# Performance work log

Measured on AMD Instinct MI355X. Metric: run time of the kernel, lower is better.

Reference implementation:

```python
import jax, jax.numpy as jnp
import numpy as np

IN_FEATURES = 512
DIM_EXPLOSION = 20
OUT_FEATURES = IN_FEATURES * DIM_EXPLOSION  # 10240
NB_PROJ_ENTRIES = 6
HASH_LENGTH = 32
BATCH = 4096


def _make_sparse_proj(key):
    """Sparse binary random projection: each of the OUT_FEATURES rows has
    NB_PROJ_ENTRIES entries set to 1 (as in OlfactoryModel.create_rand_proj_matrix)."""
    idx = jax.random.randint(key, (OUT_FEATURES, NB_PROJ_ENTRIES), 0, IN_FEATURES)
    rows = jnp.arange(OUT_FEATURES)[:, None]
    W = jnp.zeros((OUT_FEATURES, IN_FEATURES), dtype=jnp.float32)
    return W.at[rows, idx].set(1.0)


def setup_inputs() -> dict:
    key = jax.random.key(0)
    k1, k2 = jax.random.split(key)
    inp = jax.random.uniform(k1, (BATCH, IN_FEATURES), dtype=jnp.float32)
    W = _make_sparse_proj(k2)
    return {"input": inp, "weight": W, "hash_length": HASH_LENGTH}


def reference(input, weight, hash_length):
    # F.linear: [B, in] @ [out, in]^T -> [B, out]
    x = jnp.einsum('bi,oi->bo', input, weight)
    # MB_sparsify: winner-take-all, keep top `hash_length` activations per row, zero the rest
    topv = jax.lax.top_k(x, hash_length)[0]          # [B, k]
    thresh = topv[:, -1:]                            # k-th largest per row
    return jnp.where(x >= thresh, x, jnp.zeros_like(x))
```

## Files before the change

kernel.cpp:

```cpp
#include <hip/hip_runtime.h>


typedef float f4 __attribute__((ext_vector_type(4)));

constexpr int IN_F   = 512;
constexpr int OUT_F  = 10240;
constexpr int TPB    = 1024;
constexpr int ROWS   = 4;
constexpr int FPT    = OUT_F / TPB;
constexpr int NBINS  = 1024;
constexpr int CHUNK  = 8;
constexpr int NCHUNK = NBINS / CHUNK;
constexpr int NWAVES = TPB / 64;
constexpr int CAP    = 64;

__global__ __launch_bounds__(256) void extract_idx(const float* __restrict__ W,
                                                   uint4* __restrict__ packed,
                                                   int out_f) {
  int row  = blockIdx.x * 4 + (threadIdx.x >> 6);
  int lane = threadIdx.x & 63;
  if (row >= out_f) return;

  const float* wr = W + (size_t)row * IN_F;
  unsigned long long masks[8];
#pragma unroll
  for (int c = 0; c < 8; ++c) {
    float v = wr[c * 64 + lane];
    masks[c] = __ballot(v != 0.0f);
  }
  if (lane == 0) {
    unsigned idx[6] = {IN_F, IN_F, IN_F, IN_F, IN_F, IN_F};
    int n = 0;
#pragma unroll
    for (int c = 0; c < 8; ++c) {
      unsigned long long m = masks[c];
      while (m && n < 6) {
        int b = __builtin_ctzll(m);
        idx[n++] = (unsigned)(c * 64 + b);
        m &= m - 1;
      }
    }
    uint4 r;
    r.x = idx[0] | (idx[1] << 16);
    r.y = idx[2] | (idx[3] << 16);
    r.z = idx[4] | (idx[5] << 16);
    r.w = (unsigned)n;
    packed[row] = r;
  }
}

__device__ __forceinline__ float row_val(const f4* in4, uint4 p, int r) {
  const float* b = (const float*)in4;
  float s = b[(p.x & 0xFFFFu) * 4 + r];
  s += b[(p.x >> 16) * 4 + r];
  s += b[(p.y & 0xFFFFu) * 4 + r];
  s += b[(p.y >> 16) * 4 + r];
  s += b[(p.z & 0xFFFFu) * 4 + r];
  s += b[(p.z >> 16) * 4 + r];
  return s;
}

__global__ __launch_bounds__(TPB, 4) void fly_hash(const float* __restrict__ inp,
                                                   const uint4* __restrict__ packed,
                                                   const int* __restrict__ kptr,
                                                   float* __restrict__ out) {
  __shared__ f4    in4[IN_F + 1];
  __shared__ int   hist[ROWS * NBINS];
  __shared__ int   csum[ROWS * NCHUNK];
  __shared__ int   wsum[NWAVES];
  __shared__ int   sh_bstar[ROWS], sh_above[ROWS], sh_n[ROWS], sh_cnt[ROWS];
  __shared__ float sh_list[ROWS][CAP];
  __shared__ float sh_thr[ROWS];
  __shared__ int   sh_need[ROWS];

  const int tid  = threadIdx.x;
  const int lane = tid & 63;
  const int wid  = tid >> 6;
  const int row0 = blockIdx.x * ROWS;
  const int k    = *kptr;

  if (tid < IN_F) {
    const float* p = inp + (size_t)row0 * IN_F + tid;
    f4 v;
    v.x = p[0];
    v.y = p[IN_F];
    v.z = p[2 * IN_F];
    v.w = p[3 * IN_F];
    in4[tid] = v;
  } else if (tid == IN_F) {
    f4 z = {0.0f, 0.0f, 0.0f, 0.0f};
    in4[IN_F] = z;
  }
  if (tid < ROWS) { sh_bstar[tid] = -1; sh_cnt[tid] = 0; }
  for (int i = tid; i < ROWS * NBINS; i += TPB) hist[i] = 0;
  __syncthreads();

  f4 x4[FPT];
#pragma unroll
  for (int i = 0; i < FPT; ++i) {
    uint4 r = packed[tid + i * TPB];
    f4 s = in4[r.x & 0xFFFFu];
    s += in4[r.x >> 16];
    s += in4[r.y & 0xFFFFu];
    s += in4[r.y >> 16];
    s += in4[r.z & 0xFFFFu];
    s += in4[r.z >> 16];
    x4[i] = s;
#pragma unroll
    for (int rr = 0; rr < ROWS; ++rr) {
      float v = s[rr];
      if (v >= 4.0f) {
        int b = (int)((v - 4.0f) * 512.0f);
        b = b > NBINS - 1 ? NBINS - 1 : b;
        atomicAdd(&hist[rr * NBINS + b], 1);
      }
    }
  }
  __syncthreads();

  {
    const bool active = tid < ROWS * NCHUNK;
    const int r = tid >> 7;
    const int c = tid & (NCHUNK - 1);
    if (active) {
      const int base = r * NBINS + c * CHUNK;
      int ssum = 0;
#pragma unroll
      for (int j = 0; j < CHUNK; ++j) ssum += hist[base + j];
      csum[tid] = ssum;
    }
    __syncthreads();
    for (int st = 1; st < NCHUNK; st <<= 1) {
      int v = 0;
      if (active) v = csum[tid] + ((c + st < NCHUNK) ? csum[tid + st] : 0);
      __syncthreads();
      if (active) csum[tid] = v;
      __syncthreads();
    }
    if (active) {
      int above_chunk = (c + 1 < NCHUNK) ? csum[tid + 1] : 0;
      if (csum[tid] >= k && above_chunk < k) {
        int acc = above_chunk;
        int bsel = c * CHUNK, abv = above_chunk;
        for (int b = c * CHUNK + CHUNK - 1; b >= c * CHUNK; --b) {
          int h = hist[r * NBINS + b];
          if (acc + h >= k) { bsel = b; abv = acc; break; }
          acc += h;
        }
        sh_bstar[r] = bsel;
        sh_above[r] = abv;
        sh_n[r]     = hist[r * NBINS + bsel];
      }
    }
  }
  __syncthreads();

  {
    const int b0 = sh_bstar[0], b1 = sh_bstar[1];
    const int b2 = sh_bstar[2], b3 = sh_bstar[3];
#pragma unroll
    for (int i = 0; i < FPT; ++i) {
      f4 s = x4[i];
#pragma unroll
      for (int rr = 0; rr < ROWS; ++rr) {
        float v = s[rr];
        int bb = (rr == 0) ? b0 : (rr == 1) ? b1 : (rr == 2) ? b2 : b3;
        if (v >= 4.0f) {
          int b = (int)((v - 4.0f) * 512.0f);
          b = b > NBINS - 1 ? NBINS - 1 : b;
          if (b == bb) {
            int p = atomicAdd(&sh_cnt[rr], 1);
            if (p < CAP) sh_list[rr][p] = v;
          }
        }
      }
    }
  }
  __syncthreads();

  if (wid < ROWS) {
    const int r   = wid;
    const int bst = sh_bstar[r];
    const int n   = (bst >= 0) ? sh_n[r] : CAP + 1;
    if (bst >= 0 && n <= CAP && sh_cnt[r] <= CAP) {
      const int j = k - sh_above[r];
      float vl = (lane < n) ? sh_list[r][lane] : -1.0f;
      int cgt = 0, cge = 0;
      for (int m = 0; m < n; ++m) {
        float u = sh_list[r][m];
        cgt += (u > vl);
        cge += (u >= vl);
      }
      if (lane < n && cgt < j && cge >= j) sh_thr[r] = vl;
      if (lane == 0) sh_need[r] = 0;
    } else {
      if (lane == 0) sh_need[r] = 1;
    }
  }
  __syncthreads();

#pragma unroll 1
  for (int r = 0; r < ROWS; ++r) {
    if (!sh_need[r]) continue;
    unsigned lo = 0u, hi = __float_as_uint(8.0f);
    while (lo < hi) {
      unsigned mid = lo + ((hi - lo + 1u) >> 1);
      float fm = __uint_as_float(mid);
      int c = 0;
      for (int i = 0; i < FPT; ++i) {
        uint4 p = packed[tid + i * TPB];
        c += (int)__popcll(__ballot(row_val(in4, p, r) >= fm));
      }
      if (lane == 0) wsum[wid] = c;
      __syncthreads();
      int tot = 0;
#pragma unroll
      for (int w = 0; w < NWAVES; ++w) tot += wsum[w];
      if (tot >= k) lo = mid; else hi = mid - 1u;
      __syncthreads();
    }
    if (tid == 0) sh_thr[r] = __uint_as_float(lo);
    __syncthreads();
  }
  const float t0 = sh_thr[0];
  const float t1 = sh_thr[1];
  const float t2 = sh_thr[2];
  const float t3 = sh_thr[3];

  float* o0 = out + (size_t)(row0 + 0) * OUT_F;
  float* o1 = out + (size_t)(row0 + 1) * OUT_F;
  float* o2 = out + (size_t)(row0 + 2) * OUT_F;
  float* o3 = out + (size_t)(row0 + 3) * OUT_F;
#pragma unroll
  for (int i = 0; i < FPT; ++i) {
    int f = tid + i * TPB;
    f4 v = x4[i];
    __builtin_nontemporal_store((v.x >= t0) ? v.x : 0.0f, &o0[f]);
    __builtin_nontemporal_store((v.y >= t1) ? v.y : 0.0f, &o1[f]);
    __builtin_nontemporal_store((v.z >= t2) ? v.z : 0.0f, &o2[f]);
    __builtin_nontemporal_store((v.w >= t3) ? v.w : 0.0f, &o3[f]);
  }
}

extern "C" void kernel_launch(void* const* d_in, const int* in_sizes, int n_in,
                              void* d_out, int out_size, void* d_ws, size_t ws_size,
                              hipStream_t stream) {
  const float* inp = (const float*)d_in[0];
  const float* W   = (const float*)d_in[1];
  const int* kptr  = (const int*)d_in[2];
  float* out       = (float*)d_out;

  const int batch = in_sizes[0] / IN_F;
  const int out_f = in_sizes[1] / IN_F;

  uint4* packed = (uint4*)d_ws;

  hipLaunchKernelGGL(extract_idx, dim3((out_f + 3) / 4), dim3(256), 0, stream,
                     W, packed, out_f);
  hipLaunchKernelGGL(fly_hash, dim3(batch / ROWS), dim3(TPB), 0, stream,
                     inp, packed, kptr, out);
}
```

Measured before the change: 239.9 us.

## Process four row groups per block in a persistent loop

Each block now handles 16 rows as four sequential groups of 4, looping over the whole histogram/threshold pipeline per group. The grid shrinks from 1024 to 256 blocks. Before the output stores, the next group's input is loaded and the histogram reset, so the stores can overlap with that setup. The aim is to amortise block launch and setup and to let the stores run alongside the next group's work. The cost is far fewer blocks (256 on a 256-CU part, with launch bounds allowing 4 per CU), which could leave CUs idle and hurt latency hiding.

```diff
diff --git a/kernel.cpp b/kernel.cpp
--- a/kernel.cpp
+++ b/kernel.cpp
@@ -7,6 +7,7 @@
 constexpr int OUT_F  = 10240;
 constexpr int TPB    = 1024;
 constexpr int ROWS   = 4;
+constexpr int GROUPS = 4;
 constexpr int FPT    = OUT_F / TPB;
 constexpr int NBINS  = 1024;
 constexpr int CHUNK  = 8;
@@ -76,11 +77,11 @@
   const int tid  = threadIdx.x;
   const int lane = tid & 63;
   const int wid  = tid >> 6;
-  const int row0 = blockIdx.x * ROWS;
   const int k    = *kptr;
+  const int blockRow0 = blockIdx.x * (ROWS * GROUPS);
 
   if (tid < IN_F) {
-    const float* p = inp + (size_t)row0 * IN_F + tid;
+    const float* p = inp + (size_t)blockRow0 * IN_F + tid;
     f4 v;
     v.x = p[0];
     v.y = p[IN_F];
@@ -95,150 +96,173 @@
   for (int i = tid; i < ROWS * NBINS; i += TPB) hist[i] = 0;
   __syncthreads();
 
-  f4 x4[FPT];
-#pragma unroll
-  for (int i = 0; i < FPT; ++i) {
-    uint4 r = packed[tid + i * TPB];
-    f4 s = in4[r.x & 0xFFFFu];
-    s += in4[r.x >> 16];
-    s += in4[r.y & 0xFFFFu];
-    s += in4[r.y >> 16];
-    s += in4[r.z & 0xFFFFu];
-    s += in4[r.z >> 16];
-    x4[i] = s;
-#pragma unroll
-    for (int rr = 0; rr < ROWS; ++rr) {
-      float v = s[rr];
-      if (v >= 4.0f) {
-        int b = (int)((v - 4.0f) * 512.0f);
-        b = b > NBINS - 1 ? NBINS - 1 : b;
-        atomicAdd(&hist[rr * NBINS + b], 1);
-      }
-    }
-  }
-  __syncthreads();
-
-  {
-    const bool active = tid < ROWS * NCHUNK;
-    const int r = tid >> 7;
-    const int c = tid & (NCHUNK - 1);
-    if (active) {
-      const int base = r * NBINS + c * CHUNK;
-      int ssum = 0;
-#pragma unroll
-      for (int j = 0; j < CHUNK; ++j) ssum += hist[base + j];
-      csum[tid] = ssum;
-    }
-    __syncthreads();
-    for (int st = 1; st < NCHUNK; st <<= 1) {
-      int v = 0;
-      if (active) v = csum[tid] + ((c + st < NCHUNK) ? csum[tid + st] : 0);
-      __syncthreads();
-      if (active) csum[tid] = v;
-      __syncthreads();
-    }
-    if (active) {
-      int above_chunk = (c + 1 < NCHUNK) ? csum[tid + 1] : 0;
-      if (csum[tid] >= k && above_chunk < k) {
-        int acc = above_chunk;
-        int bsel = c * CHUNK, abv = above_chunk;
-        for (int b = c * CHUNK + CHUNK - 1; b >= c * CHUNK; --b) {
-          int h = hist[r * NBINS + b];
-          if (acc + h >= k) { bsel = b; abv = acc; break; }
-          acc += h;
-        }
-        sh_bstar[r] = bsel;
-        sh_above[r] = abv;
-        sh_n[r]     = hist[r * NBINS + bsel];
-      }
-    }
-  }
-  __syncthreads();
-
-  {
-    const int b0 = sh_bstar[0], b1 = sh_bstar[1];
-    const int b2 = sh_bstar[2], b3 = sh_bstar[3];
+#pragma unroll 1
+  for (int g = 0; g < GROUPS; ++g) {
+    const int row0 = blockRow0 + g * ROWS;
+
+    f4 x4[FPT];
 #pragma unroll
     for (int i = 0; i < FPT; ++i) {
-      f4 s = x4[i];
+      uint4 r = packed[tid + i * TPB];
+      f4 s = in4[r.x & 0xFFFFu];
+      s += in4[r.x >> 16];
+      s += in4[r.y & 0xFFFFu];
+      s += in4[r.y >> 16];
+      s += in4[r.z & 0xFFFFu];
+      s += in4[r.z >> 16];
+      x4[i] = s;
 #pragma unroll
       for (int rr = 0; rr < ROWS; ++rr) {
         float v = s[rr];
-        int bb = (rr == 0) ? b0 : (rr == 1) ? b1 : (rr == 2) ? b2 : b3;
         if (v >= 4.0f) {
           int b = (int)((v - 4.0f) * 512.0f);
           b = b > NBINS - 1 ? NBINS - 1 : b;
-          if (b == bb) {
-            int p = atomicAdd(&sh_cnt[rr], 1);
-            if (p < CAP) sh_list[rr][p] = v;
+          atomicAdd(&hist[rr * NBINS + b], 1);
+        }
+      }
+    }
+    __syncthreads();
+
+    {
+      const bool active = tid < ROWS * NCHUNK;
+      const int r = tid >> 7;
+      const int c = tid & (NCHUNK - 1);
+      if (active) {
+        const int base = r * NBINS + c * CHUNK;
+        int ssum = 0;
+#pragma unroll
+        for (int j = 0; j < CHUNK; ++j) ssum += hist[base + j];
+        csum[tid] = ssum;
+      }
+      __syncthreads();
+      for (int st = 1; st < NCHUNK; st <<= 1) {
+        int v = 0;
+        if (active) v = csum[tid] + ((c + st < NCHUNK) ? csum[tid + st] : 0);
+        __syncthreads();
+        if (active) csum[tid] = v;
+        __syncthreads();
+      }
+      if (active) {
+        int above_chunk = (c + 1 < NCHUNK) ? csum[tid + 1] : 0;
+        if (csum[tid] >= k && above_chunk < k) {
+          int acc = above_chunk;
+          int bsel = c * CHUNK, abv = above_chunk;
+          for (int b = c * CHUNK + CHUNK - 1; b >= c * CHUNK; --b) {
+            int h = hist[r * NBINS + b];
+            if (acc + h >= k) { bsel = b; abv = acc; break; }
+            acc += h;
           }
-        }
-      }
-    }
-  }
-  __syncthreads();
-
-  if (wid < ROWS) {
-    const int r   = wid;
-    const int bst = sh_bstar[r];
-    const int n   = (bst >= 0) ? sh_n[r] : CAP + 1;
-    if (bst >= 0 && n <= CAP && sh_cnt[r] <= CAP) {
-      const int j = k - sh_above[r];
-      float vl = (lane < n) ? sh_list[r][lane] : -1.0f;
-      int cgt = 0, cge = 0;
-      for (int m = 0; m < n; ++m) {
-        float u = sh_list[r][m];
-        cgt += (u > vl);
-        cge += (u >= vl);
-      }
-      if (lane < n && cgt < j && cge >= j) sh_thr[r] = vl;
-      if (lane == 0) sh_need[r] = 0;
-    } else {
-      if (lane == 0) sh_need[r] = 1;
-    }
-  }
-  __syncthreads();
+          sh_bstar[r] = bsel;
+          sh_above[r] = abv;
+          sh_n[r]     = hist[r * NBINS + bsel];
+        }
+      }
+    }
+    __syncthreads();
+
+    {
+      const int b0 = sh_bstar[0], b1 = sh_bstar[1];
+      const int b2 = sh_bstar[2], b3 = sh_bstar[3];
+#pragma unroll
+      for (int i = 0; i < FPT; ++i) {
+        f4 s = x4[i];
+#pragma unroll
+        for (int rr = 0; rr < ROWS; ++rr) {
+          float v = s[rr];
+          int bb = (rr == 0) ? b0 : (rr == 1) ? b1 : (rr == 2) ? b2 : b3;
+          if (v >= 4.0f) {
+            int b = (int)((v - 4.0f) * 512.0f);
+            b = b > NBINS - 1 ? NBINS - 1 : b;
+            if (b == bb) {
+              int p = atomicAdd(&sh_cnt[rr], 1);
+              if (p < CAP) sh_list[rr][p] = v;
+            }
+          }
+        }
+      }
+    }
+    __syncthreads();
+
+    if (wid < ROWS) {
+      const int r   = wid;
+      const int bst = sh_bstar[r];
+      const int n   = (bst >= 0) ? sh_n[r] : CAP + 1;
+      if (bst >= 0 && n <= CAP && sh_cnt[r] <= CAP) {
+        const int j = k - sh_above[r];
+        float vl = (lane < n) ? sh_list[r][lane] : -1.0f;
+        int cgt = 0, cge = 0;
+        for (int m = 0; m < n; ++m) {
+          float u = sh_list[r][m];
+          cgt += (u > vl);
+          cge += (u >= vl);
+        }
+        if (lane < n && cgt < j && cge >= j) sh_thr[r] = vl;
+        if (lane == 0) sh_need[r] = 0;
+      } else {
+        if (lane == 0) sh_need[r] = 1;
+      }
+    }
+    __syncthreads();
 
 #pragma unroll 1
-  for (int r = 0; r < ROWS; ++r) {
-    if (!sh_need[r]) continue;
-    unsigned lo = 0u, hi = __float_as_uint(8.0f);
-    while (lo < hi) {
-      unsigned mid = lo + ((hi - lo + 1u) >> 1);
-      float fm = __uint_as_float(mid);
-      int c = 0;
-      for (int i = 0; i < FPT; ++i) {
-        uint4 p = packed[tid + i * TPB];
-        c += (int)__popcll(__ballot(row_val(in4, p, r) >= fm));
-      }
-      if (lane == 0) wsum[wid] = c;
+    for (int r = 0; r < ROWS; ++r) {
+      if (!sh_need[r]) continue;
+      unsigned lo = 0u, hi = __float_as_uint(8.0f);
+      while (lo < hi) {
+        unsigned mid = lo + ((hi - lo + 1u) >> 1);
+        float fm = __uint_as_float(mid);
+        int c = 0;
+        for (int i = 0; i < FPT; ++i) {
+          uint4 p = packed[tid + i * TPB];
+          c += (int)__popcll(__ballot(row_val(in4, p, r) >= fm));
+        }
+        if (lane == 0) wsum[wid] = c;
+        __syncthreads();
+        int tot = 0;
+#pragma unroll
+        for (int w = 0; w < NWAVES; ++w) tot += wsum[w];
+        if (tot >= k) lo = mid; else hi = mid - 1u;
+        __syncthreads();
+      }
+      if (tid == 0) sh_thr[r] = __uint_as_float(lo);
       __syncthreads();
-      int tot = 0;
-#pragma unroll
-      for (int w = 0; w < NWAVES; ++w) tot += wsum[w];
-      if (tot >= k) lo = mid; else hi = mid - 1u;
-      __syncthreads();
-    }
-    if (tid == 0) sh_thr[r] = __uint_as_float(lo);
-    __syncthreads();
-  }
-  const float t0 = sh_thr[0];
-  const float t1 = sh_thr[1];
-  const float t2 = sh_thr[2];
-  const float t3 = sh_thr[3];
-
-  float* o0 = out + (size_t)(row0 + 0) * OUT_F;
-  float* o1 = out + (size_t)(row0 + 1) * OUT_F;
-  float* o2 = out + (size_t)(row0 + 2) * OUT_F;
-  float* o3 = out + (size_t)(row0 + 3) * OUT_F;
-#pragma unroll
-  for (int i = 0; i < FPT; ++i) {
-    int f = tid + i * TPB;
-    f4 v = x4[i];
-    __builtin_nontemporal_store((v.x >= t0) ? v.x : 0.0f, &o0[f]);
-    __builtin_nontemporal_store((v.y >= t1) ? v.y : 0.0f, &o1[f]);
-    __builtin_nontemporal_store((v.z >= t2) ? v.z : 0.0f, &o2[f]);
-    __builtin_nontemporal_store((v.w >= t3) ? v.w : 0.0f, &o3[f]);
+    }
+    const float t0 = sh_thr[0];
+    const float t1 = sh_thr[1];
+    const float t2 = sh_thr[2];
+    const float t3 = sh_thr[3];
+
+    if (g + 1 < GROUPS) {
+      if (tid < IN_F) {
+        const float* p = inp + (size_t)(row0 + ROWS) * IN_F + tid;
+        f4 v;
+        v.x = p[0];
+        v.y = p[IN_F];
+        v.z = p[2 * IN_F];
+        v.w = p[3 * IN_F];
+        in4[tid] = v;
+      } else if (tid == IN_F) {
+        f4 z = {0.0f, 0.0f, 0.0f, 0.0f};
+        in4[IN_F] = z;
+      }
+      if (tid < ROWS) { sh_bstar[tid] = -1; sh_cnt[tid] = 0; }
+      for (int i = tid; i < ROWS * NBINS; i += TPB) hist[i] = 0;
+    }
+    __syncthreads();
+
+    float* o0 = out + (size_t)(row0 + 0) * OUT_F;
+    float* o1 = out + (size_t)(row0 + 1) * OUT_F;
+    float* o2 = out + (size_t)(row0 + 2) * OUT_F;
+    float* o3 = out + (size_t)(row0 + 3) * OUT_F;
+#pragma unroll
+    for (int i = 0; i < FPT; ++i) {
+      int f = tid + i * TPB;
+      f4 v = x4[i];
+      __builtin_nontemporal_store((v.x >= t0) ? v.x : 0.0f, &o0[f]);
+      __builtin_nontemporal_store((v.y >= t1) ? v.y : 0.0f, &o1[f]);
+      __builtin_nontemporal_store((v.z >= t2) ? v.z : 0.0f, &o2[f]);
+      __builtin_nontemporal_store((v.w >= t3) ? v.w : 0.0f, &o3[f]);
+    }
   }
 }
 
@@ -257,6 +281,6 @@
 
   hipLaunchKernelGGL(extract_idx, dim3((out_f + 3) / 4), dim3(256), 0, stream,
                      W, packed, out_f);
-  hipLaunchKernelGGL(fly_hash, dim3(batch / ROWS), dim3(TPB), 0, stream,
-                     inp, packed, kptr, out);
-}
+  hipLaunchKernelGGL(fly_hash, dim3(batch / (ROWS * GROUPS)), dim3(TPB), 0,
+                     stream, inp, packed, kptr, out);
+}
```

New measurement: 285.6 us. 1.19x slower.
